# Kernel tuning notes

Measured on AMD Instinct MI355X. Metric: run time of the kernel, lower is better.

The kernel has to match this reference:

```python
import jax, jax.numpy as jnp
import numpy as np


def setup_inputs() -> dict:
    key = jax.random.key(0)
    k1, k2, k3, k4 = jax.random.split(key, 4)
    B, Nq, Nk, D = 8, 2048, 2048, 768
    return {
        "query": jax.random.normal(k1, (B, Nq, D), dtype=jnp.float32),
        "key": jax.random.normal(k2, (Nk, D), dtype=jnp.float32),
        "x": jax.random.normal(k3, (B, Nk, D), dtype=jnp.float32),
        "W": jax.random.normal(k4, (D, D), dtype=jnp.float32) * (1.0 / np.sqrt(D)),
        "b": jnp.zeros((D,), dtype=jnp.float32),
    }


def reference(query, key, x, W, b):
    # Linear projection: [B,Nq,dk] @ W^T + b -> [B,Nq,dq]
    query_proj = jnp.einsum("bqd,ed->bqe", query, W) + b
    # tensordot over dim_query: [B,Nq,dq] x [Nk,dq] -> [B,Nq,Nk]
    score = jnp.einsum("bqe,ke->bqk", query_proj, key)
    attn = jax.nn.softmax(score, axis=-1)
    # bmm: [B,Nq,Nk] @ [B,Nk,Dv] -> [B,Nq,Dv]
    out = jnp.einsum("bqk,bkd->bqd", attn, x)
    return (out, attn)
```

## Files before the change

### kernel.cpp

```cpp
#include <hip/hip_runtime.h>

typedef short s16x8 __attribute__((ext_vector_type(8)));
typedef _Float16 h16x8 __attribute__((ext_vector_type(8)));
typedef float f32x4 __attribute__((ext_vector_type(4)));

__device__ __forceinline__ unsigned short f2bf(float f) {
    unsigned int u = __builtin_bit_cast(unsigned int, f);
    u += 0x7FFFu + ((u >> 16) & 1u);
    return (unsigned short)(u >> 16);
}
__device__ __forceinline__ float bf2f(unsigned short h) {
    unsigned int u = ((unsigned int)h) << 16;
    return __builtin_bit_cast(float, u);
}
__device__ __forceinline__ unsigned short f2h(float f) {
    _Float16 h = (_Float16)f;
    return __builtin_bit_cast(unsigned short, h);
}
__device__ __forceinline__ float h2f(unsigned short u) {
    return (float)__builtin_bit_cast(_Float16, u);
}

__device__ __forceinline__ int swz(int row, int kbyte) {
    return (row * 64 + kbyte) ^ (((row >> 1) & 3) << 4);
}

__device__ __forceinline__ void gl16(const void* g, void* l) {
    __builtin_amdgcn_global_load_lds(
        (__attribute__((address_space(1))) void*)(g),
        (__attribute__((address_space(3))) void*)(l), 16, 0, 0);
}

template<int SPLIT, bool TRANSB, bool BIAS>
__global__ __launch_bounds__(256, 1) void mfma_gemm(
    const float* __restrict__ A, const float* __restrict__ Bsrc,
    const float* __restrict__ bias, float* __restrict__ C,
    int M, int N, int K, long strideA, long strideB, long strideC)
{
    constexpr int NB = (SPLIT > 1) ? 2 : 1;
    __shared__ unsigned short sA[NB][128 * 32];
    __shared__ unsigned short sB[NB][128 * 32];

    const int t  = threadIdx.x;
    const int bz = blockIdx.z;
    const float* Ab = A    + (long)bz * strideA;
    const float* Bb = Bsrc + (long)bz * strideB;
    float*       Cb = C    + (long)bz * strideC;
    const int m0 = blockIdx.y * 128;
    const int n0 = blockIdx.x * 128;

    const int l  = t & 63, w = t >> 6;
    const int rm = (w >> 1) * 64;
    const int cn = (w & 1) * 64;
    const int lr = l & 15;
    const int kg = (l >> 4) * 16;

    const int srow = t >> 1;
    const int skh  = (t & 1) * 16;
    const int s_ = t & 15;
    const int kp = t >> 4;

    f32x4 acc[4][4];
    #pragma unroll
    for (int i = 0; i < 4; ++i)
        #pragma unroll
        for (int j = 0; j < 4; ++j)
            acc[i][j] = (f32x4){0.f, 0.f, 0.f, 0.f};

    for (int kt = 0; kt < K; kt += 32) {
        {
            const float* p = &Ab[(long)(m0 + srow) * K + kt + skh];
            float f[16];
            #pragma unroll
            for (int q = 0; q < 4; ++q) {
                const float4 v = *(const float4*)(p + 4 * q);
                f[4*q+0] = v.x; f[4*q+1] = v.y; f[4*q+2] = v.z; f[4*q+3] = v.w;
            }
            s16x8 h0, h1, l0, l1;
            #pragma unroll
            for (int q = 0; q < 8; ++q) {
                unsigned short h = f2bf(f[q]);      h0[q] = (short)h;
                if (SPLIT > 1) l0[q] = (short)f2bf(f[q] - bf2f(h));
                unsigned short g = f2bf(f[8 + q]);  h1[q] = (short)g;
                if (SPLIT > 1) l1[q] = (short)f2bf(f[8 + q] - bf2f(g));
            }
            *(s16x8*)((char*)sA[0] + swz(srow, skh * 2))      = h0;
            *(s16x8*)((char*)sA[0] + swz(srow, skh * 2 + 16)) = h1;
            if (SPLIT > 1) {
                *(s16x8*)((char*)sA[1] + swz(srow, skh * 2))      = l0;
                *(s16x8*)((char*)sA[1] + swz(srow, skh * 2 + 16)) = l1;
            }
        }
        if (!TRANSB) {
            const float* p = &Bb[(long)(n0 + srow) * K + kt + skh];
            float f[16];
            #pragma unroll
            for (int q = 0; q < 4; ++q) {
                const float4 v = *(const float4*)(p + 4 * q);
                f[4*q+0] = v.x; f[4*q+1] = v.y; f[4*q+2] = v.z; f[4*q+3] = v.w;
            }
            s16x8 h0, h1, l0, l1;
            #pragma unroll
            for (int q = 0; q < 8; ++q) {
                unsigned short h = f2bf(f[q]);      h0[q] = (short)h;
                if (SPLIT > 1) l0[q] = (short)f2bf(f[q] - bf2f(h));
                unsigned short g = f2bf(f[8 + q]);  h1[q] = (short)g;
                if (SPLIT > 1) l1[q] = (short)f2bf(f[8 + q] - bf2f(g));
            }
            *(s16x8*)((char*)sB[0] + swz(srow, skh * 2))      = h0;
            *(s16x8*)((char*)sB[0] + swz(srow, skh * 2 + 16)) = h1;
            if (SPLIT > 1) {
                *(s16x8*)((char*)sB[1] + swz(srow, skh * 2))      = l0;
                *(s16x8*)((char*)sB[1] + swz(srow, skh * 2 + 16)) = l1;
            }
        } else {
            const float* r0 = &Bb[(long)(kt + 2 * kp) * N + n0 + s_ * 8];
            const float* r1 = r0 + N;
            float a0[8], a1[8];
            {
                const float4 u0 = *(const float4*)(r0);
                const float4 u1 = *(const float4*)(r0 + 4);
                const float4 v0 = *(const float4*)(r1);
                const float4 v1 = *(const float4*)(r1 + 4);
                a0[0]=u0.x;a0[1]=u0.y;a0[2]=u0.z;a0[3]=u0.w;
                a0[4]=u1.x;a0[5]=u1.y;a0[6]=u1.z;a0[7]=u1.w;
                a1[0]=v0.x;a1[1]=v0.y;a1[2]=v0.z;a1[3]=v0.w;
                a1[4]=v1.x;a1[5]=v1.y;a1[6]=v1.z;a1[7]=v1.w;
            }
            #pragma unroll
            for (int j = 0; j < 8; ++j) {
                const int i  = (j + s_) & 7;
                const int nl = s_ * 8 + i;
                const unsigned int val =
                    (unsigned int)f2bf(a0[i]) | ((unsigned int)f2bf(a1[i]) << 16);
                *(unsigned int*)((char*)sB[0] + swz(nl, 4 * kp)) = val;
            }
        }
        __syncthreads();

        s16x8 ah[4], bh[4];
        #pragma unroll
        for (int mi = 0; mi < 4; ++mi)
            ah[mi] = *(const s16x8*)((const char*)sA[0] + swz(rm + mi * 16 + lr, kg));
        #pragma unroll
        for (int nj = 0; nj < 4; ++nj)
            bh[nj] = *(const s16x8*)((const char*)sB[0] + swz(cn + nj * 16 + lr, kg));
        #pragma unroll
        for (int mi = 0; mi < 4; ++mi)
            #pragma unroll
            for (int nj = 0; nj < 4; ++nj)
                acc[mi][nj] = __builtin_amdgcn_mfma_f32_16x16x32_bf16(
                    ah[mi], bh[nj], acc[mi][nj], 0, 0, 0);
        if (SPLIT > 1) {
            s16x8 al[4], bl[4];
            #pragma unroll
            for (int mi = 0; mi < 4; ++mi)
                al[mi] = *(const s16x8*)((const char*)sA[1] + swz(rm + mi * 16 + lr, kg));
            #pragma unroll
            for (int mi = 0; mi < 4; ++mi)
                #pragma unroll
                for (int nj = 0; nj < 4; ++nj)
                    acc[mi][nj] = __builtin_amdgcn_mfma_f32_16x16x32_bf16(
                        al[mi], bh[nj], acc[mi][nj], 0, 0, 0);
            #pragma unroll
            for (int nj = 0; nj < 4; ++nj)
                bl[nj] = *(const s16x8*)((const char*)sB[1] + swz(cn + nj * 16 + lr, kg));
            #pragma unroll
            for (int mi = 0; mi < 4; ++mi)
                #pragma unroll
                for (int nj = 0; nj < 4; ++nj)
                    acc[mi][nj] = __builtin_amdgcn_mfma_f32_16x16x32_bf16(
                        ah[mi], bl[nj], acc[mi][nj], 0, 0, 0);
        }
        __syncthreads();
    }

    #pragma unroll
    for (int mi = 0; mi < 4; ++mi) {
        #pragma unroll
        for (int nj = 0; nj < 4; ++nj) {
            const int row = m0 + rm + mi * 16 + (l >> 4) * 4;
            const int col = n0 + cn + nj * 16 + lr;
            const float badd = BIAS ? bias[col] : 0.f;
            #pragma unroll
            for (int r = 0; r < 4; ++r)
                Cb[(long)(row + r) * N + col] = acc[mi][nj][r] + badd;
        }
    }
}

__global__ __launch_bounds__(256, 1) void score_gemm_f16(
    const unsigned short* __restrict__ Ah, const unsigned short* __restrict__ Al,
    const unsigned short* __restrict__ Bh,
    const float* __restrict__ bias, float* __restrict__ C,
    int M, int N, int K, int nbx)
{
    __shared__ unsigned short sAh[128 * 32];
    __shared__ unsigned short sAl[128 * 32];
    __shared__ unsigned short sBh[128 * 32];

    const int bid = blockIdx.x;
    const int cpx = gridDim.x >> 3;
    const int sw  = (bid & 7) * cpx + (bid >> 3);
    const int mb  = sw / nbx, nb = sw % nbx;
    const int m0 = mb * 128, n0 = nb * 128;

    const int t = threadIdx.x;
    const int l = t & 63, w = t >> 6;
    const int rm = (w >> 1) * 64;
    const int cn = (w & 1) * 64;
    const int lr = l & 15;
    const int kg = (l >> 4) * 16;

    const int r0 = 2 * w, r1 = 2 * w + 1;
    const int rowS0 = 16 * r0 + (l >> 2);
    const int rowS1 = 16 * r1 + (l >> 2);
    const int h0 = (l & 3) ^ ((rowS0 >> 1) & 3);
    const int h1 = (l & 3) ^ ((rowS1 >> 1) & 3);

    const unsigned short* gAh0 = Ah + (long)(m0 + rowS0) * K + 8 * h0;
    const unsigned short* gAh1 = Ah + (long)(m0 + rowS1) * K + 8 * h1;
    const unsigned short* gAl0 = Al + (long)(m0 + rowS0) * K + 8 * h0;
    const unsigned short* gAl1 = Al + (long)(m0 + rowS1) * K + 8 * h1;
    const unsigned short* gBh0 = Bh + (long)(n0 + rowS0) * K + 8 * h0;
    const unsigned short* gBh1 = Bh + (long)(n0 + rowS1) * K + 8 * h1;

    unsigned short* dA0  = &sAh[r0 * 512];
    unsigned short* dA1  = &sAh[r1 * 512];
    unsigned short* dAl0 = &sAl[r0 * 512];
    unsigned short* dAl1 = &sAl[r1 * 512];
    unsigned short* dB0  = &sBh[r0 * 512];
    unsigned short* dB1  = &sBh[r1 * 512];

    f32x4 acc[4][4];
    #pragma unroll
    for (int i = 0; i < 4; ++i)
        #pragma unroll
        for (int j = 0; j < 4; ++j)
            acc[i][j] = (f32x4){0.f, 0.f, 0.f, 0.f};

    const int nk = K >> 5;
    for (int it = 0; it < nk; ++it) {
        gl16(gAh0, dA0);  gl16(gAh1, dA1);
        gl16(gBh0, dB0);  gl16(gBh1, dB1);
        gl16(gAl0, dAl0); gl16(gAl1, dAl1);
        gAh0 += 32; gAh1 += 32; gAl0 += 32; gAl1 += 32;
        gBh0 += 32; gBh1 += 32;
        __syncthreads();

        h16x8 ah[4], bh[4];
        #pragma unroll
        for (int mi = 0; mi < 4; ++mi)
            ah[mi] = __builtin_bit_cast(h16x8,
                *(const s16x8*)((const char*)sAh + swz(rm + mi * 16 + lr, kg)));
        #pragma unroll
        for (int nj = 0; nj < 4; ++nj)
            bh[nj] = __builtin_bit_cast(h16x8,
                *(const s16x8*)((const char*)sBh + swz(cn + nj * 16 + lr, kg)));
        #pragma unroll
        for (int mi = 0; mi < 4; ++mi)
            #pragma unroll
            for (int nj = 0; nj < 4; ++nj)
                acc[mi][nj] = __builtin_amdgcn_mfma_f32_16x16x32_f16(
                    ah[mi], bh[nj], acc[mi][nj], 0, 0, 0);
        h16x8 al[4];
        #pragma unroll
        for (int mi = 0; mi < 4; ++mi)
            al[mi] = __builtin_bit_cast(h16x8,
                *(const s16x8*)((const char*)sAl + swz(rm + mi * 16 + lr, kg)));
        #pragma unroll
        for (int mi = 0; mi < 4; ++mi)
            #pragma unroll
            for (int nj = 0; nj < 4; ++nj)
                acc[mi][nj] = __builtin_amdgcn_mfma_f32_16x16x32_f16(
                    al[mi], bh[nj], acc[mi][nj], 0, 0, 0);
        __syncthreads();
    }

    #pragma unroll
    for (int mi = 0; mi < 4; ++mi) {
        #pragma unroll
        for (int nj = 0; nj < 4; ++nj) {
            const int row = m0 + rm + mi * 16 + (l >> 4) * 4;
            const int col = n0 + cn + nj * 16 + lr;
            const float badd = bias[col];
            #pragma unroll
            for (int r = 0; r < 4; ++r)
                C[(long)(row + r) * N + col] = acc[mi][nj][r] + badd;
        }
    }
}

__global__ __launch_bounds__(256, 1) void out_gemm3(
    const unsigned short* __restrict__ A16, const unsigned short* __restrict__ B16,
    float* __restrict__ C, int M, int N, int K,
    long strideA, long strideB, long strideC)
{
    __shared__ unsigned short sA[128 * 32];
    __shared__ unsigned short sB[128 * 32];

    const int bz = blockIdx.z;
    const unsigned short* Ab = A16 + (long)bz * strideA;
    const unsigned short* Bb = B16 + (long)bz * strideB;
    float* Cb = C + (long)bz * strideC;
    const int m0 = blockIdx.x * 128;
    const int n0 = blockIdx.y * 128;

    const int t = threadIdx.x;
    const int l = t & 63, w = t >> 6;
    const int rm = (w >> 1) * 64;
    const int cn = (w & 1) * 64;
    const int lr = l & 15;
    const int kg = (l >> 4) * 16;

    const int r0 = 2 * w, r1 = 2 * w + 1;
    const int rowS0 = 16 * r0 + (l >> 2);
    const int rowS1 = 16 * r1 + (l >> 2);
    const int h0 = (l & 3) ^ ((rowS0 >> 1) & 3);
    const int h1 = (l & 3) ^ ((rowS1 >> 1) & 3);

    const unsigned short* gA0 = Ab + (long)(m0 + rowS0) * K + 8 * h0;
    const unsigned short* gA1 = Ab + (long)(m0 + rowS1) * K + 8 * h1;
    const unsigned short* gB0 = Bb + (long)(n0 + rowS0) * K + 8 * h0;
    const unsigned short* gB1 = Bb + (long)(n0 + rowS1) * K + 8 * h1;
    unsigned short* dA0 = &sA[r0 * 512];
    unsigned short* dA1 = &sA[r1 * 512];
    unsigned short* dB0 = &sB[r0 * 512];
    unsigned short* dB1 = &sB[r1 * 512];

    f32x4 acc[4][4];
    #pragma unroll
    for (int i = 0; i < 4; ++i)
        #pragma unroll
        for (int j = 0; j < 4; ++j)
            acc[i][j] = (f32x4){0.f, 0.f, 0.f, 0.f};

    const int nk = K >> 5;
    for (int it = 0; it < nk; ++it) {
        gl16(gA0, dA0); gl16(gA1, dA1);
        gl16(gB0, dB0); gl16(gB1, dB1);
        gA0 += 32; gA1 += 32; gB0 += 32; gB1 += 32;
        __syncthreads();

        h16x8 ah[4], bh[4];
        #pragma unroll
        for (int mi = 0; mi < 4; ++mi)
            ah[mi] = __builtin_bit_cast(h16x8,
                *(const s16x8*)((const char*)sA + swz(rm + mi * 16 + lr, kg)));
        #pragma unroll
        for (int nj = 0; nj < 4; ++nj)
            bh[nj] = __builtin_bit_cast(h16x8,
                *(const s16x8*)((const char*)sB + swz(cn + nj * 16 + lr, kg)));
        #pragma unroll
        for (int mi = 0; mi < 4; ++mi)
            #pragma unroll
            for (int nj = 0; nj < 4; ++nj)
                acc[mi][nj] = __builtin_amdgcn_mfma_f32_16x16x32_f16(
                    ah[mi], bh[nj], acc[mi][nj], 0, 0, 0);
        __syncthreads();
    }

    #pragma unroll
    for (int mi = 0; mi < 4; ++mi) {
        #pragma unroll
        for (int nj = 0; nj < 4; ++nj) {
            const int row = m0 + rm + mi * 16 + (l >> 4) * 4;
            const int col = n0 + cn + nj * 16 + lr;
            #pragma unroll
            for (int r = 0; r < 4; ++r)
                Cb[(long)(row + r) * N + col] = acc[mi][nj][r];
        }
    }
}

__global__ __launch_bounds__(256, 1) void out_gemm(
    const float* __restrict__ A32, const unsigned short* __restrict__ B16,
    float* __restrict__ C, int M, int N, int K,
    long strideA, long strideB, long strideC)
{
    __shared__ unsigned short sA[128 * 32];
    __shared__ unsigned short sB[128 * 32];

    const int bz = blockIdx.z;
    const float* Ab = A32 + (long)bz * strideA;
    const unsigned short* Bb = B16 + (long)bz * strideB;
    float* Cb = C + (long)bz * strideC;
    const int m0 = blockIdx.x * 128;
    const int n0 = blockIdx.y * 128;

    const int t = threadIdx.x;
    const int l = t & 63, w = t >> 6;
    const int rm = (w >> 1) * 64;
    const int cn = (w & 1) * 64;
    const int lr = l & 15;
    const int kg = (l >> 4) * 16;

    const int r0 = 2 * w, r1 = 2 * w + 1;
    const int rowS0 = 16 * r0 + (l >> 2);
    const int rowS1 = 16 * r1 + (l >> 2);
    const int h0 = (l & 3) ^ ((rowS0 >> 1) & 3);
    const int h1 = (l & 3) ^ ((rowS1 >> 1) & 3);
    const unsigned short* gB0 = Bb + (long)(n0 + rowS0) * K + 8 * h0;
    const unsigned short* gB1 = Bb + (long)(n0 + rowS1) * K + 8 * h1;
    unsigned short* dB0 = &sB[r0 * 512];
    unsigned short* dB1 = &sB[r1 * 512];

    const int srow = t >> 1;
    const int skh  = (t & 1) * 16;
    const float* gA = &Ab[(long)(m0 + srow) * K + skh];

    f32x4 acc[4][4];
    #pragma unroll
    for (int i = 0; i < 4; ++i)
        #pragma unroll
        for (int j = 0; j < 4; ++j)
            acc[i][j] = (f32x4){0.f, 0.f, 0.f, 0.f};

    const int nk = K >> 5;
    for (int it = 0; it < nk; ++it) {
        gl16(gB0, dB0); gl16(gB1, dB1);
        gB0 += 32; gB1 += 32;
        {
            float f[16];
            #pragma unroll
            for (int q = 0; q < 4; ++q) {
                const float4 v = *(const float4*)(gA + 4 * q);
                f[4*q+0] = v.x; f[4*q+1] = v.y; f[4*q+2] = v.z; f[4*q+3] = v.w;
            }
            gA += 32;
            s16x8 v0, v1;
            #pragma unroll
            for (int q = 0; q < 8; ++q) {
                v0[q] = (short)f2bf(f[q]);
                v1[q] = (short)f2bf(f[8 + q]);
            }
            *(s16x8*)((char*)sA + swz(srow, skh * 2))      = v0;
            *(s16x8*)((char*)sA + swz(srow, skh * 2 + 16)) = v1;
        }
        __syncthreads();

        s16x8 ah[4], bh[4];
        #pragma unroll
        for (int mi = 0; mi < 4; ++mi)
            ah[mi] = *(const s16x8*)((const char*)sA + swz(rm + mi * 16 + lr, kg));
        #pragma unroll
        for (int nj = 0; nj < 4; ++nj)
            bh[nj] = *(const s16x8*)((const char*)sB + swz(cn + nj * 16 + lr, kg));
        #pragma unroll
        for (int mi = 0; mi < 4; ++mi)
            #pragma unroll
            for (int nj = 0; nj < 4; ++nj)
                acc[mi][nj] = __builtin_amdgcn_mfma_f32_16x16x32_bf16(
                    ah[mi], bh[nj], acc[mi][nj], 0, 0, 0);
        __syncthreads();
    }

    #pragma unroll
    for (int mi = 0; mi < 4; ++mi) {
        #pragma unroll
        for (int nj = 0; nj < 4; ++nj) {
            const int row = m0 + rm + mi * 16 + (l >> 4) * 4;
            const int col = n0 + cn + nj * 16 + lr;
            #pragma unroll
            for (int r = 0; r < 4; ++r)
                Cb[(long)(row + r) * N + col] = acc[mi][nj][r];
        }
    }
}

__global__ __launch_bounds__(256, 1) void score_gemm(
    const unsigned short* __restrict__ Ah, const unsigned short* __restrict__ Al,
    const unsigned short* __restrict__ Bh, const unsigned short* __restrict__ Bl,
    const float* __restrict__ bias, float* __restrict__ C,
    int M, int N, int K, int nbx)
{
    __shared__ unsigned short sAh[128 * 32];
    __shared__ unsigned short sBh[128 * 32];
    __shared__ unsigned short sAl[128 * 32];
    __shared__ unsigned short sBl[128 * 32];

    const int bid = blockIdx.x;
    const int cpx = gridDim.x >> 3;
    const int sw  = (bid & 7) * cpx + (bid >> 3);
    const int mb  = sw / nbx, nb = sw % nbx;
    const int m0 = mb * 128, n0 = nb * 128;

    const int t = threadIdx.x;
    const int l = t & 63, w = t >> 6;
    const int rm = (w >> 1) * 64;
    const int cn = (w & 1) * 64;
    const int lr = l & 15;
    const int kg = (l >> 4) * 16;

    const int r0 = 2 * w, r1 = 2 * w + 1;
    const int rowS0 = 16 * r0 + (l >> 2);
    const int rowS1 = 16 * r1 + (l >> 2);
    const int h0 = (l & 3) ^ ((rowS0 >> 1) & 3);
    const int h1 = (l & 3) ^ ((rowS1 >> 1) & 3);

    const unsigned short* gAh0 = Ah + (long)(m0 + rowS0) * K + 8 * h0;
    const unsigned short* gAh1 = Ah + (long)(m0 + rowS1) * K + 8 * h1;
    const unsigned short* gAl0 = Al + (long)(m0 + rowS0) * K + 8 * h0;
    const unsigned short* gAl1 = Al + (long)(m0 + rowS1) * K + 8 * h1;
    const unsigned short* gBh0 = Bh + (long)(n0 + rowS0) * K + 8 * h0;
    const unsigned short* gBh1 = Bh + (long)(n0 + rowS1) * K + 8 * h1;
    const unsigned short* gBl0 = Bl + (long)(n0 + rowS0) * K + 8 * h0;
    const unsigned short* gBl1 = Bl + (long)(n0 + rowS1) * K + 8 * h1;

    unsigned short* dA0 = &sAh[r0 * 512];
    unsigned short* dA1 = &sAh[r1 * 512];
    unsigned short* dAl0 = &sAl[r0 * 512];
    unsigned short* dAl1 = &sAl[r1 * 512];
    unsigned short* dB0 = &sBh[r0 * 512];
    unsigned short* dB1 = &sBh[r1 * 512];
    unsigned short* dBl0 = &sBl[r0 * 512];
    unsigned short* dBl1 = &sBl[r1 * 512];

    f32x4 acc[4][4];
    #pragma unroll
    for (int i = 0; i < 4; ++i)
        #pragma unroll
        for (int j = 0; j < 4; ++j)
            acc[i][j] = (f32x4){0.f, 0.f, 0.f, 0.f};

    const int nk = K >> 5;
    for (int it = 0; it < nk; ++it) {
        gl16(gAh0, dA0);  gl16(gAh1, dA1);
        gl16(gBh0, dB0);  gl16(gBh1, dB1);
        gl16(gAl0, dAl0); gl16(gAl1, dAl1);
        gl16(gBl0, dBl0); gl16(gBl1, dBl1);
        gAh0 += 32; gAh1 += 32; gAl0 += 32; gAl1 += 32;
        gBh0 += 32; gBh1 += 32; gBl0 += 32; gBl1 += 32;
        __syncthreads();

        s16x8 ah[4], bh[4];
        #pragma unroll
        for (int mi = 0; mi < 4; ++mi)
            ah[mi] = *(const s16x8*)((const char*)sAh + swz(rm + mi * 16 + lr, kg));
        #pragma unroll
        for (int nj = 0; nj < 4; ++nj)
            bh[nj] = *(const s16x8*)((const char*)sBh + swz(cn + nj * 16 + lr, kg));
        #pragma unroll
        for (int mi = 0; mi < 4; ++mi)
            #pragma unroll
            for (int nj = 0; nj < 4; ++nj)
                acc[mi][nj] = __builtin_amdgcn_mfma_f32_16x16x32_bf16(
                    ah[mi], bh[nj], acc[mi][nj], 0, 0, 0);
        s16x8 al[4], bl[4];
        #pragma unroll
        for (int mi = 0; mi < 4; ++mi)
            al[mi] = *(const s16x8*)((const char*)sAl + swz(rm + mi * 16 + lr, kg));
        #pragma unroll
        for (int mi = 0; mi < 4; ++mi)
            #pragma unroll
            for (int nj = 0; nj < 4; ++nj)
                acc[mi][nj] = __builtin_amdgcn_mfma_f32_16x16x32_bf16(
                    al[mi], bh[nj], acc[mi][nj], 0, 0, 0);
        #pragma unroll
        for (int nj = 0; nj < 4; ++nj)
            bl[nj] = *(const s16x8*)((const char*)sBl + swz(cn + nj * 16 + lr, kg));
        #pragma unroll
        for (int mi = 0; mi < 4; ++mi)
            #pragma unroll
            for (int nj = 0; nj < 4; ++nj)
                acc[mi][nj] = __builtin_amdgcn_mfma_f32_16x16x32_bf16(
                    ah[mi], bl[nj], acc[mi][nj], 0, 0, 0);
        __syncthreads();
    }

    #pragma unroll
    for (int mi = 0; mi < 4; ++mi) {
        #pragma unroll
        for (int nj = 0; nj < 4; ++nj) {
            const int row = m0 + rm + mi * 16 + (l >> 4) * 4;
            const int col = n0 + cn + nj * 16 + lr;
            const float badd = bias[col];
            #pragma unroll
            for (int r = 0; r < 4; ++r)
                C[(long)(row + r) * N + col] = acc[mi][nj][r] + badd;
        }
    }
}

template<int MODE>
__global__ __launch_bounds__(256) void transpose64(
    const float* __restrict__ in, void* __restrict__ outv,
    int R, int Cc, long sIn, long sOut)
{
    __shared__ float tl[64][65];
    const int z = blockIdx.z;
    const float* ib = in + (long)z * sIn;
    const int r0 = blockIdx.x * 64, c0 = blockIdx.y * 64;
    const int t = threadIdx.x;
    const int lrr = t >> 4, lc = (t & 15) * 4;
    #pragma unroll
    for (int p = 0; p < 4; ++p) {
        const float4 v = *(const float4*)&ib[(long)(r0 + lrr + 16 * p) * Cc + c0 + lc];
        tl[lrr + 16 * p][lc + 0] = v.x; tl[lrr + 16 * p][lc + 1] = v.y;
        tl[lrr + 16 * p][lc + 2] = v.z; tl[lrr + 16 * p][lc + 3] = v.w;
    }
    __syncthreads();
    #pragma unroll
    for (int p = 0; p < 4; ++p) {
        const int orow = c0 + lrr + 16 * p;
        const int ocol = r0 + lc;
        const float a = tl[lc + 0][lrr + 16 * p];
        const float b = tl[lc + 1][lrr + 16 * p];
        const float c = tl[lc + 2][lrr + 16 * p];
        const float d = tl[lc + 3][lrr + 16 * p];
        if (MODE == 1) {
            ushort4 u = { f2bf(a), f2bf(b), f2bf(c), f2bf(d) };
            *(ushort4*)((unsigned short*)outv + (long)z * sOut + (long)orow * R + ocol) = u;
        } else if (MODE == 2) {
            ushort4 u = { f2h(a), f2h(b), f2h(c), f2h(d) };
            *(ushort4*)((unsigned short*)outv + (long)z * sOut + (long)orow * R + ocol) = u;
        } else {
            float4 u = { a, b, c, d };
            *(float4*)((float*)outv + (long)z * sOut + (long)orow * R + ocol) = u;
        }
    }
}

__global__ __launch_bounds__(256) void convert_hilo(
    const float* __restrict__ src, unsigned short* __restrict__ hi,
    unsigned short* __restrict__ lo, long n8)
{
    for (long i = (long)blockIdx.x * blockDim.x + threadIdx.x; i < n8;
         i += (long)gridDim.x * blockDim.x) {
        const float4 a = *(const float4*)&src[i * 8];
        const float4 b = *(const float4*)&src[i * 8 + 4];
        const float f[8] = { a.x, a.y, a.z, a.w, b.x, b.y, b.z, b.w };
        s16x8 h, lv;
        #pragma unroll
        for (int q = 0; q < 8; ++q) {
            const unsigned short hh = f2bf(f[q]);
            h[q]  = (short)hh;
            lv[q] = (short)f2bf(f[q] - bf2f(hh));
        }
        *(s16x8*)&hi[i * 8] = h;
        *(s16x8*)&lo[i * 8] = lv;
    }
}

__global__ __launch_bounds__(256) void convert_hilo_f16(
    const float* __restrict__ src, unsigned short* __restrict__ hi,
    unsigned short* __restrict__ lo, long n8)
{
    for (long i = (long)blockIdx.x * blockDim.x + threadIdx.x; i < n8;
         i += (long)gridDim.x * blockDim.x) {
        const float4 a = *(const float4*)&src[i * 8];
        const float4 b = *(const float4*)&src[i * 8 + 4];
        const float f[8] = { a.x, a.y, a.z, a.w, b.x, b.y, b.z, b.w };
        s16x8 h, lv;
        #pragma unroll
        for (int q = 0; q < 8; ++q) {
            const unsigned short hh = f2h(f[q]);
            h[q]  = (short)hh;
            lv[q] = (short)f2h(f[q] - h2f(hh));
        }
        *(s16x8*)&hi[i * 8] = h;
        *(s16x8*)&lo[i * 8] = lv;
    }
}

__global__ __launch_bounds__(256) void bk_dot(
    const float* __restrict__ key, const float* __restrict__ b,
    float* __restrict__ bk, int D)
{
    const int row = blockIdx.x * 4 + (threadIdx.x >> 6);
    const int l = threadIdx.x & 63;
    const float* kr = key + (long)row * D;
    float s = 0.f;
    for (int e = l; e < D; e += 64) s += kr[e] * b[e];
    #pragma unroll
    for (int off = 32; off > 0; off >>= 1) s += __shfl_xor(s, off);
    if (l == 0) bk[row] = s;
}

__global__ __launch_bounds__(256) void softmax_f16(
    float* __restrict__ S, unsigned short* __restrict__ S16, int cols)
{
    const long row = blockIdx.x;
    float* p = S + row * (long)cols;
    unsigned short* p16 = S16 + row * (long)cols;
    const int t = threadIdx.x;
    const int wid = t >> 6;
    const int base = t * 8;

    const float4 a = *(const float4*)&p[base];
    const float4 b = *(const float4*)&p[base + 4];
    float vals[8] = { a.x, a.y, a.z, a.w, b.x, b.y, b.z, b.w };
    float m = -INFINITY;
    #pragma unroll
    for (int i = 0; i < 8; ++i) m = fmaxf(m, vals[i]);
    #pragma unroll
    for (int off = 32; off > 0; off >>= 1)
        m = fmaxf(m, __shfl_xor(m, off));
    __shared__ float smax[4], ssum[4];
    if ((t & 63) == 0) smax[wid] = m;
    __syncthreads();
    m = fmaxf(fmaxf(smax[0], smax[1]), fmaxf(smax[2], smax[3]));

    float s = 0.f;
    #pragma unroll
    for (int i = 0; i < 8; ++i) {
        vals[i] = __expf(vals[i] - m);
        s += vals[i];
    }
    #pragma unroll
    for (int off = 32; off > 0; off >>= 1)
        s += __shfl_xor(s, off);
    if ((t & 63) == 0) ssum[wid] = s;
    __syncthreads();
    s = (ssum[0] + ssum[1]) + (ssum[2] + ssum[3]);
    const float inv = 1.0f / s;

    float4 o0, o1;
    o0.x = vals[0]*inv; o0.y = vals[1]*inv; o0.z = vals[2]*inv; o0.w = vals[3]*inv;
    o1.x = vals[4]*inv; o1.y = vals[5]*inv; o1.z = vals[6]*inv; o1.w = vals[7]*inv;
    *(float4*)&p[base]     = o0;
    *(float4*)&p[base + 4] = o1;
    s16x8 h;
    h[0]=(short)f2h(o0.x); h[1]=(short)f2h(o0.y); h[2]=(short)f2h(o0.z); h[3]=(short)f2h(o0.w);
    h[4]=(short)f2h(o1.x); h[5]=(short)f2h(o1.y); h[6]=(short)f2h(o1.z); h[7]=(short)f2h(o1.w);
    *(s16x8*)&p16[base] = h;
}

__global__ __launch_bounds__(256) void softmax_rows(float* __restrict__ S, int cols)
{
    const long row = blockIdx.x;
    float* p = S + row * (long)cols;
    const int t = threadIdx.x;
    const int wid = t >> 6;

    float vals[8];
    float m = -INFINITY;
    #pragma unroll
    for (int i = 0; i < 8; ++i) {
        vals[i] = p[t + i * 256];
        m = fmaxf(m, vals[i]);
    }
    #pragma unroll
    for (int off = 32; off > 0; off >>= 1)
        m = fmaxf(m, __shfl_xor(m, off));
    __shared__ float smax[4], ssum[4];
    if ((t & 63) == 0) smax[wid] = m;
    __syncthreads();
    m = fmaxf(fmaxf(smax[0], smax[1]), fmaxf(smax[2], smax[3]));

    float s = 0.f;
    #pragma unroll
    for (int i = 0; i < 8; ++i) {
        vals[i] = __expf(vals[i] - m);
        s += vals[i];
    }
    #pragma unroll
    for (int off = 32; off > 0; off >>= 1)
        s += __shfl_xor(s, off);
    if ((t & 63) == 0) ssum[wid] = s;
    __syncthreads();
    s = (ssum[0] + ssum[1]) + (ssum[2] + ssum[3]);
    const float inv = 1.0f / s;
    #pragma unroll
    for (int i = 0; i < 8; ++i)
        p[t + i * 256] = vals[i] * inv;
}

extern "C" void kernel_launch(void* const* d_in, const int* in_sizes, int n_in,
                              void* d_out, int out_size, void* d_ws, size_t ws_size,
                              hipStream_t stream)
{
    const float* query = (const float*)d_in[0];
    const float* key   = (const float*)d_in[1];
    const float* x     = (const float*)d_in[2];
    const float* W     = (const float*)d_in[3];
    const float* bias  = (const float*)d_in[4];

    const int D  = in_sizes[4];
    const int Nk = in_sizes[1] / D;
    const int B  = in_sizes[2] / (Nk * D);
    const int Nq = in_sizes[0] / (B * D);

    float* out  = (float*)d_out;
    float* attn = out + (long)B * Nq * D;

    const long nQ  = (long)B * Nq * D;
    const long nKW = (long)Nk * D;
    const long nX  = (long)B * Nk * D;

    const size_t xTb   = (size_t)nX * 2;
    const size_t qLob  = (size_t)nQ * 2;
    const size_t atb1  = (size_t)Nq * Nk * 2;
    const size_t wsMin = xTb + qLob;

    int g = 0;
    if (ws_size >= wsMin) {
        g = (int)((ws_size - xTb) / atb1);
        if (g > B) g = B;
    }

    if (g >= 2) {
        unsigned short* q_hi  = (unsigned short*)out;
        unsigned short* KW_hi = q_hi + nQ;
        unsigned short* KW_lo = KW_hi + nKW;
        float*          bk    = (float*)(KW_lo + nKW);
        unsigned short* xT     = (unsigned short*)d_ws;
        unsigned short* q_lo   = (unsigned short*)((char*)d_ws + xTb);
        unsigned short* attn16 = (unsigned short*)((char*)d_ws + xTb);
        float* Wt  = attn;
        float* KWf = attn + 1048576;

        dim3 gtw(D / 64, D / 64, 1);
        transpose64<0><<<gtw, 256, 0, stream>>>(W, Wt, D, D, 0L, 0L);
        dim3 gkw(D / 128, Nk / 128, 1);
        mfma_gemm<3, false, false><<<gkw, 256, 0, stream>>>(
            key, Wt, nullptr, KWf, Nk, D, D, 0L, 0L, 0L);
        convert_hilo_f16<<<768, 256, 0, stream>>>(KWf, KW_hi, KW_lo, nKW / 8);
        bk_dot<<<Nk / 4, 256, 0, stream>>>(key, bias, bk, D);
        convert_hilo_f16<<<2048, 256, 0, stream>>>(query, q_hi, q_lo, nQ / 8);
        dim3 gtx(Nk / 64, D / 64, B);
        transpose64<2><<<gtx, 256, 0, stream>>>(
            x, xT, Nk, D, (long)Nk * D, (long)D * Nk);
        const int nbx = Nk / 128;
        const int nwg = (B * Nq / 128) * nbx;
        score_gemm_f16<<<nwg, 256, 0, stream>>>(
            q_hi, q_lo, KW_hi, bk, attn, B * Nq, Nk, D, nbx);

        for (int b0 = 0; b0 < B; b0 += g) {
            const int gb = (b0 + g <= B) ? g : (B - b0);
            softmax_f16<<<gb * Nq, 256, 0, stream>>>(
                attn + (long)b0 * Nq * Nk, attn16, Nk);
            dim3 go(Nq / 128, D / 128, gb);
            out_gemm3<<<go, 256, 0, stream>>>(
                attn16, xT + (long)b0 * D * Nk, out + (long)b0 * Nq * D,
                Nq, D, Nk, (long)Nq * Nk, (long)D * Nk, (long)Nq * D);
        }
    } else if (ws_size >= wsMin) {
        unsigned short* q_hi  = (unsigned short*)out;
        unsigned short* KW_hi = q_hi + nQ;
        unsigned short* KW_lo = KW_hi + nKW;
        float*          bk    = (float*)(KW_lo + nKW);
        unsigned short* q_lo  = (unsigned short*)d_ws;
        unsigned short* xT    = q_lo + nQ;
        float* Wt  = attn;
        float* KWf = attn + 1048576;

        dim3 gtw(D / 64, D / 64, 1);
        transpose64<0><<<gtw, 256, 0, stream>>>(W, Wt, D, D, 0L, 0L);
        dim3 gkw(D / 128, Nk / 128, 1);
        mfma_gemm<3, false, false><<<gkw, 256, 0, stream>>>(
            key, Wt, nullptr, KWf, Nk, D, D, 0L, 0L, 0L);
        convert_hilo<<<768, 256, 0, stream>>>(KWf, KW_hi, KW_lo, nKW / 8);
        bk_dot<<<Nk / 4, 256, 0, stream>>>(key, bias, bk, D);
        convert_hilo<<<2048, 256, 0, stream>>>(query, q_hi, q_lo, nQ / 8);
        dim3 gtx(Nk / 64, D / 64, B);
        transpose64<1><<<gtx, 256, 0, stream>>>(
            x, xT, Nk, D, (long)Nk * D, (long)D * Nk);
        const int nbx = Nk / 128;
        const int nwg = (B * Nq / 128) * nbx;
        score_gemm<<<nwg, 256, 0, stream>>>(
            q_hi, q_lo, KW_hi, KW_lo, bk, attn, B * Nq, Nk, D, nbx);
        softmax_rows<<<B * Nq, 256, 0, stream>>>(attn, Nk);
        dim3 go(Nq / 128, D / 128, B);
        out_gemm<<<go, 256, 0, stream>>>(
            attn, xT, out, Nq, D, Nk, (long)Nq * Nk, (long)D * Nk, (long)Nq * D);
    } else {
        float* qp = out;
        dim3 g1(D / 128, (B * Nq) / 128, 1);
        mfma_gemm<3, false, true><<<g1, 256, 0, stream>>>(
            query, W, bias, qp, B * Nq, D, D, 0L, 0L, 0L);
        dim3 g2(Nk / 128, Nq / 128, B);
        mfma_gemm<3, false, false><<<g2, 256, 0, stream>>>(
            qp, key, nullptr, attn, Nq, Nk, D, (long)Nq * D, 0L, (long)Nq * Nk);
        softmax_rows<<<B * Nq, 256, 0, stream>>>(attn, Nk);
        dim3 g4(D / 128, Nq / 128, B);
        mfma_gemm<1, true, false><<<g4, 256, 0, stream>>>(
            attn, x, nullptr, out, Nq, D, Nk, (long)Nq * Nk, (long)Nk * D, (long)Nq * D);
    }
}
```

Baseline: 352.4 us.

## Add double-buffered 64-K GEMMs with interleaved hi/lo query layout

Replaces the score and PV GEMMs with kernels that double-buffer LDS tiles of depth 64 and prefetch the next tile while MFMAs run, so there is one barrier per iteration instead of two. The score GEMM now runs as a single K=2D GEMM: query hi and lo halves are interleaved per row, and KW is duplicated, which replaces the separate hi/lo operand streams. This needs extra workspace for the duplicated KW and bias, which can reduce the batch group size g. It also uses more LDS per block.

```diff
diff --git a/kernel.cpp b/kernel.cpp
--- a/kernel.cpp
+++ b/kernel.cpp
@@ -29,6 +29,201 @@
     __builtin_amdgcn_global_load_lds(
         (__attribute__((address_space(1))) void*)(g),
         (__attribute__((address_space(3))) void*)(l), 16, 0, 0);
+}
+
+
+__global__ __launch_bounds__(256, 1) void score_2ph(
+    const unsigned short* __restrict__ A, const unsigned short* __restrict__ Bm,
+    const float* __restrict__ bias, float* __restrict__ C,
+    int M, int N, int K, int nbx)
+{
+    __shared__ unsigned short lds[2][2][128 * 64];
+
+    const int bid = blockIdx.x;
+    const int cpx = gridDim.x >> 3;
+    const int sw  = (bid & 7) * cpx + (bid >> 3);
+    const int m0 = (sw / nbx) * 128, n0 = (sw % nbx) * 128;
+
+    const int t = threadIdx.x;
+    const int l = t & 63, w = t >> 6;
+    const int rm = (w >> 1) * 64, cn = (w & 1) * 64;
+    const int lr = l & 15;
+    const int kg16 = (l >> 4) * 16;
+
+    const int jrow   = l >> 3;
+    const int srcoff = ((l & 7) ^ jrow) << 3;
+
+    const unsigned short* gA = A  + (long)(m0 + jrow) * K + srcoff;
+    const unsigned short* gB = Bm + (long)(n0 + jrow) * K + srcoff;
+
+    f32x4 acc[4][4];
+    #pragma unroll
+    for (int i = 0; i < 4; ++i)
+        #pragma unroll
+        for (int j = 0; j < 4; ++j)
+            acc[i][j] = (f32x4){0.f, 0.f, 0.f, 0.f};
+
+    const int nt = K >> 6;
+    #pragma unroll
+    for (int i = 0; i < 4; ++i) {
+        const int c = w * 4 + i;
+        gl16(gA + (long)(8 * c) * K, &lds[0][0][c * 512]);
+        gl16(gB + (long)(8 * c) * K, &lds[0][1][c * 512]);
+    }
+    __syncthreads();
+
+    int p = 0;
+    for (int it = 0; it < nt; ++it) {
+        if (it + 1 < nt) {
+            const unsigned short* nA = gA + (it + 1) * 64;
+            const unsigned short* nB = gB + (it + 1) * 64;
+            #pragma unroll
+            for (int i = 0; i < 4; ++i) {
+                const int c = w * 4 + i;
+                gl16(nA + (long)(8 * c) * K, &lds[p ^ 1][0][c * 512]);
+                gl16(nB + (long)(8 * c) * K, &lds[p ^ 1][1][c * 512]);
+            }
+        }
+        const char* baseA = (const char*)&lds[p][0][0];
+        const char* baseB = (const char*)&lds[p][1][0];
+        h16x8 af[2][4], bf[2][4];
+        #pragma unroll
+        for (int ks = 0; ks < 2; ++ks)
+            #pragma unroll
+            for (int mi = 0; mi < 4; ++mi) {
+                const int row = rm + mi * 16 + lr;
+                af[ks][mi] = *(const h16x8*)(baseA + row * 128 +
+                                ((ks * 64 + kg16) ^ ((row & 7) << 4)));
+            }
+        #pragma unroll
+        for (int ks = 0; ks < 2; ++ks)
+            #pragma unroll
+            for (int nj = 0; nj < 4; ++nj) {
+                const int row = cn + nj * 16 + lr;
+                bf[ks][nj] = *(const h16x8*)(baseB + row * 128 +
+                                ((ks * 64 + kg16) ^ ((row & 7) << 4)));
+            }
+        #pragma unroll
+        for (int ks = 0; ks < 2; ++ks)
+            #pragma unroll
+            for (int mi = 0; mi < 4; ++mi)
+                #pragma unroll
+                for (int nj = 0; nj < 4; ++nj)
+                    acc[mi][nj] = __builtin_amdgcn_mfma_f32_16x16x32_f16(
+                        af[ks][mi], bf[ks][nj], acc[mi][nj], 0, 0, 0);
+        __syncthreads();
+        p ^= 1;
+    }
+
+    #pragma unroll
+    for (int mi = 0; mi < 4; ++mi) {
+        #pragma unroll
+        for (int nj = 0; nj < 4; ++nj) {
+            const int row = m0 + rm + mi * 16 + (l >> 4) * 4;
+            const int col = n0 + cn + nj * 16 + lr;
+            const float badd = bias[col];
+            #pragma unroll
+            for (int r = 0; r < 4; ++r)
+                C[(long)(row + r) * N + col] = acc[mi][nj][r] + badd;
+        }
+    }
+}
+
+__global__ __launch_bounds__(256, 1) void pv_2ph(
+    const unsigned short* __restrict__ A, const unsigned short* __restrict__ Bm,
+    float* __restrict__ C, int M, int N, int K,
+    long strideA, long strideB, long strideC)
+{
+    __shared__ unsigned short lds[2][2][128 * 64];
+
+    const int bz = blockIdx.z;
+    const unsigned short* Ab = A  + (long)bz * strideA;
+    const unsigned short* Bb = Bm + (long)bz * strideB;
+    float* Cb = C + (long)bz * strideC;
+    const int m0 = blockIdx.x * 128, n0 = blockIdx.y * 128;
+
+    const int t = threadIdx.x;
+    const int l = t & 63, w = t >> 6;
+    const int rm = (w >> 1) * 64, cn = (w & 1) * 64;
+    const int lr = l & 15;
+    const int kg16 = (l >> 4) * 16;
+
+    const int jrow   = l >> 3;
+    const int srcoff = ((l & 7) ^ jrow) << 3;
+
+    const unsigned short* gA = Ab + (long)(m0 + jrow) * K + srcoff;
+    const unsigned short* gB = Bb + (long)(n0 + jrow) * K + srcoff;
+
+    f32x4 acc[4][4];
+    #pragma unroll
+    for (int i = 0; i < 4; ++i)
+        #pragma unroll
+        for (int j = 0; j < 4; ++j)
+            acc[i][j] = (f32x4){0.f, 0.f, 0.f, 0.f};
+
+    const int nt = K >> 6;
+    #pragma unroll
+    for (int i = 0; i < 4; ++i) {
+        const int c = w * 4 + i;
+        gl16(gA + (long)(8 * c) * K, &lds[0][0][c * 512]);
+        gl16(gB + (long)(8 * c) * K, &lds[0][1][c * 512]);
+    }
+    __syncthreads();
+
+    int p = 0;
+    for (int it = 0; it < nt; ++it) {
+        if (it + 1 < nt) {
+            const unsigned short* nA = gA + (it + 1) * 64;
+            const unsigned short* nB = gB + (it + 1) * 64;
+            #pragma unroll
+            for (int i = 0; i < 4; ++i) {
+                const int c = w * 4 + i;
+                gl16(nA + (long)(8 * c) * K, &lds[p ^ 1][0][c * 512]);
+                gl16(nB + (long)(8 * c) * K, &lds[p ^ 1][1][c * 512]);
+            }
+        }
+        const char* baseA = (const char*)&lds[p][0][0];
+        const char* baseB = (const char*)&lds[p][1][0];
+        h16x8 af[2][4], bf[2][4];
+        #pragma unroll
+        for (int ks = 0; ks < 2; ++ks)
+            #pragma unroll
+            for (int mi = 0; mi < 4; ++mi) {
+                const int row = rm + mi * 16 + lr;
+                af[ks][mi] = *(const h16x8*)(baseA + row * 128 +
+                                ((ks * 64 + kg16) ^ ((row & 7) << 4)));
+            }
+        #pragma unroll
+        for (int ks = 0; ks < 2; ++ks)
+            #pragma unroll
+            for (int nj = 0; nj < 4; ++nj) {
+                const int row = cn + nj * 16 + lr;
+                bf[ks][nj] = *(const h16x8*)(baseB + row * 128 +
+                                ((ks * 64 + kg16) ^ ((row & 7) << 4)));
+            }
+        #pragma unroll
+        for (int ks = 0; ks < 2; ++ks)
+            #pragma unroll
+            for (int mi = 0; mi < 4; ++mi)
+                #pragma unroll
+                for (int nj = 0; nj < 4; ++nj)
+                    acc[mi][nj] = __builtin_amdgcn_mfma_f32_16x16x32_f16(
+                        af[ks][mi], bf[ks][nj], acc[mi][nj], 0, 0, 0);
+        __syncthreads();
+        p ^= 1;
+    }
+
+    #pragma unroll
+    for (int mi = 0; mi < 4; ++mi) {
+        #pragma unroll
+        for (int nj = 0; nj < 4; ++nj) {
+            const int row = m0 + rm + mi * 16 + (l >> 4) * 4;
+            const int col = n0 + cn + nj * 16 + lr;
+            #pragma unroll
+            for (int r = 0; r < 4; ++r)
+                Cb[(long)(row + r) * N + col] = acc[mi][nj][r];
+        }
+    }
 }
 
 template<int SPLIT, bool TRANSB, bool BIAS>
@@ -189,15 +384,16 @@
     }
 }
 
-__global__ __launch_bounds__(256, 1) void score_gemm_f16(
+__global__ __launch_bounds__(256, 1) void score_gemm(
     const unsigned short* __restrict__ Ah, const unsigned short* __restrict__ Al,
-    const unsigned short* __restrict__ Bh,
+    const unsigned short* __restrict__ Bh, const unsigned short* __restrict__ Bl,
     const float* __restrict__ bias, float* __restrict__ C,
     int M, int N, int K, int nbx)
 {
     __shared__ unsigned short sAh[128 * 32];
+    __shared__ unsigned short sBh[128 * 32];
     __shared__ unsigned short sAl[128 * 32];
-    __shared__ unsigned short sBh[128 * 32];
+    __shared__ unsigned short sBl[128 * 32];
 
     const int bid = blockIdx.x;
     const int cpx = gridDim.x >> 3;
@@ -224,13 +420,17 @@
     const unsigned short* gAl1 = Al + (long)(m0 + rowS1) * K + 8 * h1;
     const unsigned short* gBh0 = Bh + (long)(n0 + rowS0) * K + 8 * h0;
     const unsigned short* gBh1 = Bh + (long)(n0 + rowS1) * K + 8 * h1;
-
-    unsigned short* dA0  = &sAh[r0 * 512];
-    unsigned short* dA1  = &sAh[r1 * 512];
+    const unsigned short* gBl0 = Bl + (long)(n0 + rowS0) * K + 8 * h0;
+    const unsigned short* gBl1 = Bl + (long)(n0 + rowS1) * K + 8 * h1;
+
+    unsigned short* dA0 = &sAh[r0 * 512];
+    unsigned short* dA1 = &sAh[r1 * 512];
     unsigned short* dAl0 = &sAl[r0 * 512];
     unsigned short* dAl1 = &sAl[r1 * 512];
-    unsigned short* dB0  = &sBh[r0 * 512];
-    unsigned short* dB1  = &sBh[r1 * 512];
+    unsigned short* dB0 = &sBh[r0 * 512];
+    unsigned short* dB1 = &sBh[r1 * 512];
+    unsigned short* dBl0 = &sBl[r0 * 512];
+    unsigned short* dBl1 = &sBl[r1 * 512];
 
     f32x4 acc[4][4];
     #pragma unroll
@@ -244,36 +444,43 @@
         gl16(gAh0, dA0);  gl16(gAh1, dA1);
         gl16(gBh0, dB0);  gl16(gBh1, dB1);
         gl16(gAl0, dAl0); gl16(gAl1, dAl1);
+        gl16(gBl0, dBl0); gl16(gBl1, dBl1);
         gAh0 += 32; gAh1 += 32; gAl0 += 32; gAl1 += 32;
-        gBh0 += 32; gBh1 += 32;
+        gBh0 += 32; gBh1 += 32; gBl0 += 32; gBl1 += 32;
         __syncthreads();
 
-        h16x8 ah[4], bh[4];
+        s16x8 ah[4], bh[4];
         #pragma unroll
         for (int mi = 0; mi < 4; ++mi)
-            ah[mi] = __builtin_bit_cast(h16x8,
-                *(const s16x8*)((const char*)sAh + swz(rm + mi * 16 + lr, kg)));
+            ah[mi] = *(const s16x8*)((const char*)sAh + swz(rm + mi * 16 + lr, kg));
         #pragma unroll
         for (int nj = 0; nj < 4; ++nj)
-            bh[nj] = __builtin_bit_cast(h16x8,
-                *(const s16x8*)((const char*)sBh + swz(cn + nj * 16 + lr, kg)));
+            bh[nj] = *(const s16x8*)((const char*)sBh + swz(cn + nj * 16 + lr, kg));
         #pragma unroll
         for (int mi = 0; mi < 4; ++mi)
             #pragma unroll
             for (int nj = 0; nj < 4; ++nj)
-                acc[mi][nj] = __builtin_amdgcn_mfma_f32_16x16x32_f16(
+                acc[mi][nj] = __builtin_amdgcn_mfma_f32_16x16x32_bf16(
                     ah[mi], bh[nj], acc[mi][nj], 0, 0, 0);
-        h16x8 al[4];
+        s16x8 al[4], bl[4];
         #pragma unroll
         for (int mi = 0; mi < 4; ++mi)
-            al[mi] = __builtin_bit_cast(h16x8,
-                *(const s16x8*)((const char*)sAl + swz(rm + mi * 16 + lr, kg)));
+            al[mi] = *(const s16x8*)((const char*)sAl + swz(rm + mi * 16 + lr, kg));
         #pragma unroll
         for (int mi = 0; mi < 4; ++mi)
             #pragma unroll
             for (int nj = 0; nj < 4; ++nj)
-                acc[mi][nj] = __builtin_amdgcn_mfma_f32_16x16x32_f16(
+                acc[mi][nj] = __builtin_amdgcn_mfma_f32_16x16x32_bf16(
                     al[mi], bh[nj], acc[mi][nj], 0, 0, 0);
+        #pragma unroll
+        for (int nj = 0; nj < 4; ++nj)
+            bl[nj] = *(const s16x8*)((const char*)sBl + swz(cn + nj * 16 + lr, kg));
+        #pragma unroll
+        for (int mi = 0; mi < 4; ++mi)
+            #pragma unroll
+            for (int nj = 0; nj < 4; ++nj)
+                acc[mi][nj] = __builtin_amdgcn_mfma_f32_16x16x32_bf16(
+                    ah[mi], bl[nj], acc[mi][nj], 0, 0, 0);
         __syncthreads();
     }
 
@@ -287,88 +494,6 @@
             #pragma unroll
             for (int r = 0; r < 4; ++r)
                 C[(long)(row + r) * N + col] = acc[mi][nj][r] + badd;
-        }
-    }
-}
-
-__global__ __launch_bounds__(256, 1) void out_gemm3(
-    const unsigned short* __restrict__ A16, const unsigned short* __restrict__ B16,
-    float* __restrict__ C, int M, int N, int K,
-    long strideA, long strideB, long strideC)
-{
-    __shared__ unsigned short sA[128 * 32];
-    __shared__ unsigned short sB[128 * 32];
-
-    const int bz = blockIdx.z;
-    const unsigned short* Ab = A16 + (long)bz * strideA;
-    const unsigned short* Bb = B16 + (long)bz * strideB;
-    float* Cb = C + (long)bz * strideC;
-    const int m0 = blockIdx.x * 128;
-    const int n0 = blockIdx.y * 128;
-
-    const int t = threadIdx.x;
-    const int l = t & 63, w = t >> 6;
-    const int rm = (w >> 1) * 64;
-    const int cn = (w & 1) * 64;
-    const int lr = l & 15;
-    const int kg = (l >> 4) * 16;
-
-    const int r0 = 2 * w, r1 = 2 * w + 1;
-    const int rowS0 = 16 * r0 + (l >> 2);
-    const int rowS1 = 16 * r1 + (l >> 2);
-    const int h0 = (l & 3) ^ ((rowS0 >> 1) & 3);
-    const int h1 = (l & 3) ^ ((rowS1 >> 1) & 3);
-
-    const unsigned short* gA0 = Ab + (long)(m0 + rowS0) * K + 8 * h0;
-    const unsigned short* gA1 = Ab + (long)(m0 + rowS1) * K + 8 * h1;
-    const unsigned short* gB0 = Bb + (long)(n0 + rowS0) * K + 8 * h0;
-    const unsigned short* gB1 = Bb + (long)(n0 + rowS1) * K + 8 * h1;
-    unsigned short* dA0 = &sA[r0 * 512];
-    unsigned short* dA1 = &sA[r1 * 512];
-    unsigned short* dB0 = &sB[r0 * 512];
-    unsigned short* dB1 = &sB[r1 * 512];
-
-    f32x4 acc[4][4];
-    #pragma unroll
-    for (int i = 0; i < 4; ++i)
-        #pragma unroll
-        for (int j = 0; j < 4; ++j)
-            acc[i][j] = (f32x4){0.f, 0.f, 0.f, 0.f};
-
-    const int nk = K >> 5;
-    for (int it = 0; it < nk; ++it) {
-        gl16(gA0, dA0); gl16(gA1, dA1);
-        gl16(gB0, dB0); gl16(gB1, dB1);
-        gA0 += 32; gA1 += 32; gB0 += 32; gB1 += 32;
-        __syncthreads();
-
-        h16x8 ah[4], bh[4];
-        #pragma unroll
-        for (int mi = 0; mi < 4; ++mi)
-            ah[mi] = __builtin_bit_cast(h16x8,
-                *(const s16x8*)((const char*)sA + swz(rm + mi * 16 + lr, kg)));
-        #pragma unroll
-        for (int nj = 0; nj < 4; ++nj)
-            bh[nj] = __builtin_bit_cast(h16x8,
-                *(const s16x8*)((const char*)sB + swz(cn + nj * 16 + lr, kg)));
-        #pragma unroll
-        for (int mi = 0; mi < 4; ++mi)
-            #pragma unroll
-            for (int nj = 0; nj < 4; ++nj)
-                acc[mi][nj] = __builtin_amdgcn_mfma_f32_16x16x32_f16(
-                    ah[mi], bh[nj], acc[mi][nj], 0, 0, 0);
-        __syncthreads();
-    }
-
-    #pragma unroll
-    for (int mi = 0; mi < 4; ++mi) {
-        #pragma unroll
-        for (int nj = 0; nj < 4; ++nj) {
-            const int row = m0 + rm + mi * 16 + (l >> 4) * 4;
-            const int col = n0 + cn + nj * 16 + lr;
-            #pragma unroll
-            for (int r = 0; r < 4; ++r)
-                Cb[(long)(row + r) * N + col] = acc[mi][nj][r];
         }
     }
 }
@@ -464,120 +589,6 @@
             #pragma unroll
             for (int r = 0; r < 4; ++r)
                 Cb[(long)(row + r) * N + col] = acc[mi][nj][r];
-        }
-    }
-}
-
-__global__ __launch_bounds__(256, 1) void score_gemm(
-    const unsigned short* __restrict__ Ah, const unsigned short* __restrict__ Al,
-    const unsigned short* __restrict__ Bh, const unsigned short* __restrict__ Bl,
-    const float* __restrict__ bias, float* __restrict__ C,
-    int M, int N, int K, int nbx)
-{
-    __shared__ unsigned short sAh[128 * 32];
-    __shared__ unsigned short sBh[128 * 32];
-    __shared__ unsigned short sAl[128 * 32];
-    __shared__ unsigned short sBl[128 * 32];
-
-    const int bid = blockIdx.x;
-    const int cpx = gridDim.x >> 3;
-    const int sw  = (bid & 7) * cpx + (bid >> 3);
-    const int mb  = sw / nbx, nb = sw % nbx;
-    const int m0 = mb * 128, n0 = nb * 128;
-
-    const int t = threadIdx.x;
-    const int l = t & 63, w = t >> 6;
-    const int rm = (w >> 1) * 64;
-    const int cn = (w & 1) * 64;
-    const int lr = l & 15;
-    const int kg = (l >> 4) * 16;
-
-    const int r0 = 2 * w, r1 = 2 * w + 1;
-    const int rowS0 = 16 * r0 + (l >> 2);
-    const int rowS1 = 16 * r1 + (l >> 2);
-    const int h0 = (l & 3) ^ ((rowS0 >> 1) & 3);
-    const int h1 = (l & 3) ^ ((rowS1 >> 1) & 3);
-
-    const unsigned short* gAh0 = Ah + (long)(m0 + rowS0) * K + 8 * h0;
-    const unsigned short* gAh1 = Ah + (long)(m0 + rowS1) * K + 8 * h1;
-    const unsigned short* gAl0 = Al + (long)(m0 + rowS0) * K + 8 * h0;
-    const unsigned short* gAl1 = Al + (long)(m0 + rowS1) * K + 8 * h1;
-    const unsigned short* gBh0 = Bh + (long)(n0 + rowS0) * K + 8 * h0;
-    const unsigned short* gBh1 = Bh + (long)(n0 + rowS1) * K + 8 * h1;
-    const unsigned short* gBl0 = Bl + (long)(n0 + rowS0) * K + 8 * h0;
-    const unsigned short* gBl1 = Bl + (long)(n0 + rowS1) * K + 8 * h1;
-
-    unsigned short* dA0 = &sAh[r0 * 512];
-    unsigned short* dA1 = &sAh[r1 * 512];
-    unsigned short* dAl0 = &sAl[r0 * 512];
-    unsigned short* dAl1 = &sAl[r1 * 512];
-    unsigned short* dB0 = &sBh[r0 * 512];
-    unsigned short* dB1 = &sBh[r1 * 512];
-    unsigned short* dBl0 = &sBl[r0 * 512];
-    unsigned short* dBl1 = &sBl[r1 * 512];
-
-    f32x4 acc[4][4];
-    #pragma unroll
-    for (int i = 0; i < 4; ++i)
-        #pragma unroll
-        for (int j = 0; j < 4; ++j)
-            acc[i][j] = (f32x4){0.f, 0.f, 0.f, 0.f};
-
-    const int nk = K >> 5;
-    for (int it = 0; it < nk; ++it) {
-        gl16(gAh0, dA0);  gl16(gAh1, dA1);
-        gl16(gBh0, dB0);  gl16(gBh1, dB1);
-        gl16(gAl0, dAl0); gl16(gAl1, dAl1);
-        gl16(gBl0, dBl0); gl16(gBl1, dBl1);
-        gAh0 += 32; gAh1 += 32; gAl0 += 32; gAl1 += 32;
-        gBh0 += 32; gBh1 += 32; gBl0 += 32; gBl1 += 32;
-        __syncthreads();
-
-        s16x8 ah[4], bh[4];
-        #pragma unroll
-        for (int mi = 0; mi < 4; ++mi)
-            ah[mi] = *(const s16x8*)((const char*)sAh + swz(rm + mi * 16 + lr, kg));
-        #pragma unroll
-        for (int nj = 0; nj < 4; ++nj)
-            bh[nj] = *(const s16x8*)((const char*)sBh + swz(cn + nj * 16 + lr, kg));
-        #pragma unroll
-        for (int mi = 0; mi < 4; ++mi)
-            #pragma unroll
-            for (int nj = 0; nj < 4; ++nj)
-                acc[mi][nj] = __builtin_amdgcn_mfma_f32_16x16x32_bf16(
-                    ah[mi], bh[nj], acc[mi][nj], 0, 0, 0);
-        s16x8 al[4], bl[4];
-        #pragma unroll
-        for (int mi = 0; mi < 4; ++mi)
-            al[mi] = *(const s16x8*)((const char*)sAl + swz(rm + mi * 16 + lr, kg));
-        #pragma unroll
-        for (int mi = 0; mi < 4; ++mi)
-            #pragma unroll
-            for (int nj = 0; nj < 4; ++nj)
-                acc[mi][nj] = __builtin_amdgcn_mfma_f32_16x16x32_bf16(
-                    al[mi], bh[nj], acc[mi][nj], 0, 0, 0);
-        #pragma unroll
-        for (int nj = 0; nj < 4; ++nj)
-            bl[nj] = *(const s16x8*)((const char*)sBl + swz(cn + nj * 16 + lr, kg));
-        #pragma unroll
-        for (int mi = 0; mi < 4; ++mi)
-            #pragma unroll
-            for (int nj = 0; nj < 4; ++nj)
-                acc[mi][nj] = __builtin_amdgcn_mfma_f32_16x16x32_bf16(
-                    ah[mi], bl[nj], acc[mi][nj], 0, 0, 0);
-        __syncthreads();
-    }
-
-    #pragma unroll
-    for (int mi = 0; mi < 4; ++mi) {
-        #pragma unroll
-        for (int nj = 0; nj < 4; ++nj) {
-            const int row = m0 + rm + mi * 16 + (l >> 4) * 4;
-            const int col = n0 + cn + nj * 16 + lr;
-            const float badd = bias[col];
-            #pragma unroll
-            for (int r = 0; r < 4; ++r)
-                C[(long)(row + r) * N + col] = acc[mi][nj][r] + badd;
         }
     }
 }
@@ -642,12 +653,15 @@
     }
 }
 
-__global__ __launch_bounds__(256) void convert_hilo_f16(
-    const float* __restrict__ src, unsigned short* __restrict__ hi,
-    unsigned short* __restrict__ lo, long n8)
-{
+__global__ __launch_bounds__(256) void convert_q_ilv(
+    const float* __restrict__ src, unsigned short* __restrict__ dst,
+    int kd8, long n8)
+{
+    const int Kd = kd8 * 8;
     for (long i = (long)blockIdx.x * blockDim.x + threadIdx.x; i < n8;
          i += (long)gridDim.x * blockDim.x) {
+        const long row = i / kd8;
+        const int  col = (int)(i - row * kd8) * 8;
         const float4 a = *(const float4*)&src[i * 8];
         const float4 b = *(const float4*)&src[i * 8 + 4];
         const float f[8] = { a.x, a.y, a.z, a.w, b.x, b.y, b.z, b.w };
@@ -658,8 +672,30 @@
             h[q]  = (short)hh;
             lv[q] = (short)f2h(f[q] - h2f(hh));
         }
-        *(s16x8*)&hi[i * 8] = h;
-        *(s16x8*)&lo[i * 8] = lv;
+        unsigned short* dr = dst + row * (long)(2 * Kd);
+        *(s16x8*)&dr[col]      = h;
+        *(s16x8*)&dr[Kd + col] = lv;
+    }
+}
+
+__global__ __launch_bounds__(256) void convert_kw_dup(
+    const float* __restrict__ src, unsigned short* __restrict__ dst,
+    int kd8, long n8)
+{
+    const int Kd = kd8 * 8;
+    for (long i = (long)blockIdx.x * blockDim.x + threadIdx.x; i < n8;
+         i += (long)gridDim.x * blockDim.x) {
+        const long row = i / kd8;
+        const int  col = (int)(i - row * kd8) * 8;
+        const float4 a = *(const float4*)&src[i * 8];
+        const float4 b = *(const float4*)&src[i * 8 + 4];
+        const float f[8] = { a.x, a.y, a.z, a.w, b.x, b.y, b.z, b.w };
+        s16x8 h;
+        #pragma unroll
+        for (int q = 0; q < 8; ++q) h[q] = (short)f2h(f[q]);
+        unsigned short* dr = dst + row * (long)(2 * Kd);
+        *(s16x8*)&dr[col]      = h;
+        *(s16x8*)&dr[Kd + col] = h;
     }
 }
 
@@ -787,26 +823,29 @@
     const long nQ  = (long)B * Nq * D;
     const long nKW = (long)Nk * D;
     const long nX  = (long)B * Nk * D;
-
-    const size_t xTb   = (size_t)nX * 2;
-    const size_t qLob  = (size_t)nQ * 2;
-    const size_t atb1  = (size_t)Nq * Nk * 2;
-    const size_t wsMin = xTb + qLob;
+    const int  M   = B * Nq;
+    const int  K2  = 2 * D;
+
+    const size_t xTb    = (size_t)nX * 2;
+    const size_t kwDupB = (size_t)Nk * K2 * 2;
+    const size_t bkB    = (size_t)Nk * 4;
+    const size_t atb1   = (size_t)Nq * Nk * 2;
+    const size_t fixedB = xTb + kwDupB + bkB;
+    const size_t qLob   = (size_t)nQ * 2;
+    const size_t wsMid  = xTb + qLob;
 
     int g = 0;
-    if (ws_size >= wsMin) {
-        g = (int)((ws_size - xTb) / atb1);
+    if (ws_size >= fixedB + 2 * atb1) {
+        g = (int)((ws_size - fixedB) / atb1);
         if (g > B) g = B;
     }
 
     if (g >= 2) {
-        unsigned short* q_hi  = (unsigned short*)out;
-        unsigned short* KW_hi = q_hi + nQ;
-        unsigned short* KW_lo = KW_hi + nKW;
-        float*          bk    = (float*)(KW_lo + nKW);
+        unsigned short* qIlv  = (unsigned short*)out;
         unsigned short* xT     = (unsigned short*)d_ws;
-        unsigned short* q_lo   = (unsigned short*)((char*)d_ws + xTb);
-        unsigned short* attn16 = (unsigned short*)((char*)d_ws + xTb);
+        unsigned short* kwDup  = (unsigned short*)((char*)d_ws + xTb);
+        float*          bk     = (float*)((char*)d_ws + xTb + kwDupB);
+        unsigned short* attn16 = (unsigned short*)((char*)d_ws + fixedB);
         float* Wt  = attn;
         float* KWf = attn + 1048576;
 
@@ -815,27 +854,28 @@
         dim3 gkw(D / 128, Nk / 128, 1);
         mfma_gemm<3, false, false><<<gkw, 256, 0, stream>>>(
             key, Wt, nullptr, KWf, Nk, D, D, 0L, 0L, 0L);
-        convert_hilo_f16<<<768, 256, 0, stream>>>(KWf, KW_hi, KW_lo, nKW / 8);
+        convert_kw_dup<<<768, 256, 0, stream>>>(KWf, kwDup, D / 8, nKW / 8);
         bk_dot<<<Nk / 4, 256, 0, stream>>>(key, bias, bk, D);
-        convert_hilo_f16<<<2048, 256, 0, stream>>>(query, q_hi, q_lo, nQ / 8);
+        convert_q_ilv<<<2048, 256, 0, stream>>>(query, qIlv, D / 8, nQ / 8);
         dim3 gtx(Nk / 64, D / 64, B);
         transpose64<2><<<gtx, 256, 0, stream>>>(
             x, xT, Nk, D, (long)Nk * D, (long)D * Nk);
+
         const int nbx = Nk / 128;
-        const int nwg = (B * Nq / 128) * nbx;
-        score_gemm_f16<<<nwg, 256, 0, stream>>>(
-            q_hi, q_lo, KW_hi, bk, attn, B * Nq, Nk, D, nbx);
+        const int nwg = (M / 128) * nbx;
+        score_2ph<<<nwg, 256, 0, stream>>>(
+            qIlv, kwDup, bk, attn, M, Nk, K2, nbx);
 
         for (int b0 = 0; b0 < B; b0 += g) {
             const int gb = (b0 + g <= B) ? g : (B - b0);
             softmax_f16<<<gb * Nq, 256, 0, stream>>>(
                 attn + (long)b0 * Nq * Nk, attn16, Nk);
             dim3 go(Nq / 128, D / 128, gb);
-            out_gemm3<<<go, 256, 0, stream>>>(
+            pv_2ph<<<go, 256, 0, stream>>>(
                 attn16, xT + (long)b0 * D * Nk, out + (long)b0 * Nq * D,
                 Nq, D, Nk, (long)Nq * Nk, (long)D * Nk, (long)Nq * D);
         }
-    } else if (ws_size >= wsMin) {
+    } else if (ws_size >= wsMid) {
         unsigned short* q_hi  = (unsigned short*)out;
         unsigned short* KW_hi = q_hi + nQ;
         unsigned short* KW_lo = KW_hi + nKW;
```

Result: no change. 347.9 us (-1.3%).
